# Kernel optimization log

Hardware: AMD Instinct MI355X
Metric: run time of the kernel (lower is better)

The kernel has to match this reference:

```python
import jax, jax.numpy as jnp
import numpy as np

HID = 32
NUM_GRAPHS = 256
N_NODES = 100000


def graph_conv(x, src, dst, ew, rel_w, rel_b, root_w):
    # PyG GraphConv: out = lin_rel(sum_{j in N(i)} e_ji * x_j) + lin_root(x_i)
    msg = x[src] * ew[:, None]                                  # [E, F] gather
    agg = jax.ops.segment_sum(msg, dst, num_segments=N_NODES)    # [N, F] scatter-add
    return agg @ rel_w + rel_b + x @ root_w


def setup_inputs() -> dict:
    key = jax.random.key(0)
    ks = jax.random.split(key, 16)
    N, E, F = N_NODES, 1600000, 64
    x = jax.random.normal(ks[0], (N, F), dtype=jnp.float32)
    edge_index = jax.random.randint(ks[1], (2, E), 0, N, dtype=jnp.int64)
    edge_attr = jax.random.uniform(ks[2], (E,), dtype=jnp.float32)
    batch = jnp.sort(jax.random.randint(ks[3], (N,), 0, NUM_GRAPHS, dtype=jnp.int64))
    s = lambda k, shp: jax.random.normal(k, shp, dtype=jnp.float32) * 0.1
    return {
        "x": x, "edge_index": edge_index, "edge_attr": edge_attr, "batch": batch,
        "conv1_rel_w": s(ks[4], (F, HID)), "conv1_rel_b": jnp.zeros((HID,), jnp.float32),
        "conv1_root_w": s(ks[5], (F, HID)),
        "conv2_rel_w": s(ks[6], (HID, HID)), "conv2_rel_b": jnp.zeros((HID,), jnp.float32),
        "conv2_root_w": s(ks[7], (HID, HID)),
        "lin1_w": s(ks[8], (HID, 32)), "lin1_b": jnp.zeros((32,), jnp.float32),
        "lin2_w": s(ks[9], (32, 16)), "lin2_b": jnp.zeros((16,), jnp.float32),
        "lin_w": s(ks[10], (16, 1)), "lin_b": jnp.zeros((1,), jnp.float32),
    }


def reference(x, edge_index, edge_attr, batch,
              conv1_rel_w, conv1_rel_b, conv1_root_w,
              conv2_rel_w, conv2_rel_b, conv2_root_w,
              lin1_w, lin1_b, lin2_w, lin2_b, lin_w, lin_b):
    src, dst = edge_index[0], edge_index[1]
    h = jax.nn.relu(graph_conv(x, src, dst, edge_attr, conv1_rel_w, conv1_rel_b, conv1_root_w))
    h = jax.nn.relu(graph_conv(h, src, dst, edge_attr, conv2_rel_w, conv2_rel_b, conv2_root_w))
    # global mean pool over graphs
    sums = jax.ops.segment_sum(h, batch, num_segments=NUM_GRAPHS)          # [G, 32]
    cnts = jax.ops.segment_sum(jnp.ones((h.shape[0],), h.dtype), batch, num_segments=NUM_GRAPHS)
    g = sums / jnp.maximum(cnts, 1.0)[:, None]
    # dropout is identity in eval mode
    g = jax.nn.relu(g @ lin1_w + lin1_b)
    g = g @ lin2_w + lin2_b
    g = jax.nn.relu(g)
    return g @ lin_w + lin_b  # [G, 1]
```

## Files before the change

kernel.cpp:

```cpp
#include <hip/hip_runtime.h>

#define NGRAPH 256
#define FIN 64
#define HID 32
#define NB_SHIFT 8
#define NB_NODES 256
#define KMAX2 512
#define EPB 2048
#define EPT 8
#define NT 64
#define XPAD 65
#define HPAD 33

__global__ __launch_bounds__(256, 4) void node_lin64(
    const float* __restrict__ x, const float* __restrict__ Wrel,
    const float* __restrict__ Wroot, const float* __restrict__ bias,
    float* __restrict__ A, float* __restrict__ B, int N)
{
    __shared__ float sWr[FIN * HID];
    __shared__ float sWo[FIN * HID];
    __shared__ float sb[HID];
    __shared__ float sx[NT * XPAD];
    int tid = threadIdx.x;
    {
        const float4* Wr4 = (const float4*)Wrel;
        const float4* Wo4 = (const float4*)Wroot;
        for (int i = tid; i < FIN * HID / 4; i += 256) {
            ((float4*)sWr)[i] = Wr4[i];
            ((float4*)sWo)[i] = Wo4[i];
        }
        if (tid < HID) sb[tid] = bias[tid];
    }
    int base = blockIdx.x * NT;
    {
        const float4* x4 = (const float4*)x;
        for (int i = tid; i < NT * 16; i += 256) {
            int row = i >> 4, c4 = i & 15;
            int n = base + row;
            float4 v = (n < N) ? x4[(size_t)n * 16 + c4]
                               : make_float4(0.f, 0.f, 0.f, 0.f);
            *(float4*)&sx[row * XPAD + c4 * 4] = v;
        }
    }
    __syncthreads();

    int nl = tid >> 3;
    int fq = (tid & 7) * 4;
    const float* xa = &sx[nl * XPAD];
    const float* xb = &sx[(nl + 32) * XPAD];
    float4 ar0 = make_float4(0.f,0.f,0.f,0.f), ao0 = ar0;
    float4 ar1 = ar0, ao1 = ar0;
    #pragma unroll 4
    for (int k = 0; k < FIN; ++k) {
        float4 w4 = *(const float4*)&sWr[k * HID + fq];
        float4 o4 = *(const float4*)&sWo[k * HID + fq];
        float va = xa[k], vb = xb[k];
        ar0.x = fmaf(va, w4.x, ar0.x); ar0.y = fmaf(va, w4.y, ar0.y);
        ar0.z = fmaf(va, w4.z, ar0.z); ar0.w = fmaf(va, w4.w, ar0.w);
        ao0.x = fmaf(va, o4.x, ao0.x); ao0.y = fmaf(va, o4.y, ao0.y);
        ao0.z = fmaf(va, o4.z, ao0.z); ao0.w = fmaf(va, o4.w, ao0.w);
        ar1.x = fmaf(vb, w4.x, ar1.x); ar1.y = fmaf(vb, w4.y, ar1.y);
        ar1.z = fmaf(vb, w4.z, ar1.z); ar1.w = fmaf(vb, w4.w, ar1.w);
        ao1.x = fmaf(vb, o4.x, ao1.x); ao1.y = fmaf(vb, o4.y, ao1.y);
        ao1.z = fmaf(vb, o4.z, ao1.z); ao1.w = fmaf(vb, o4.w, ao1.w);
    }
    float4 bb = *(const float4*)&sb[fq];
    int n0 = base + nl, n1 = base + nl + 32;
    if (n0 < N) {
        *(float4*)&A[(size_t)n0 * HID + fq] = ar0;
        ao0.x += bb.x; ao0.y += bb.y; ao0.z += bb.z; ao0.w += bb.w;
        *(float4*)&B[(size_t)n0 * HID + fq] = ao0;
    }
    if (n1 < N) {
        *(float4*)&A[(size_t)n1 * HID + fq] = ar1;
        ao1.x += bb.x; ao1.y += bb.y; ao1.z += bb.z; ao1.w += bb.w;
        *(float4*)&B[(size_t)n1 * HID + fq] = ao1;
    }
}

__global__ __launch_bounds__(256, 4) void node_lin32(
    const float* __restrict__ Hpre, const float* __restrict__ Wrel,
    const float* __restrict__ Wroot, const float* __restrict__ bias,
    float* __restrict__ A, float* __restrict__ C, int N)
{
    __shared__ float sWr[HID * HID];
    __shared__ float sWo[HID * HID];
    __shared__ float sb[HID];
    __shared__ float sh[NT * HPAD];
    int tid = threadIdx.x;
    {
        const float4* Wr4 = (const float4*)Wrel;
        const float4* Wo4 = (const float4*)Wroot;
        for (int i = tid; i < HID * HID / 4; i += 256) {
            ((float4*)sWr)[i] = Wr4[i];
            ((float4*)sWo)[i] = Wo4[i];
        }
        if (tid < HID) sb[tid] = bias[tid];
    }
    int base = blockIdx.x * NT;
    {
        const float4* H4 = (const float4*)Hpre;
        for (int i = tid; i < NT * 8; i += 256) {
            int row = i >> 3, c4 = i & 7;
            int n = base + row;
            float4 v = make_float4(0.f, 0.f, 0.f, 0.f);
            if (n < N) {
                v = H4[(size_t)n * 8 + c4];
                v.x = v.x > 0.f ? v.x : 0.f; v.y = v.y > 0.f ? v.y : 0.f;
                v.z = v.z > 0.f ? v.z : 0.f; v.w = v.w > 0.f ? v.w : 0.f;
            }
            *(float4*)&sh[row * HPAD + c4 * 4] = v;
        }
    }
    __syncthreads();

    int nl = tid >> 3;
    int fq = (tid & 7) * 4;
    const float* xa = &sh[nl * HPAD];
    const float* xb = &sh[(nl + 32) * HPAD];
    float4 ar0 = make_float4(0.f,0.f,0.f,0.f), ao0 = ar0;
    float4 ar1 = ar0, ao1 = ar0;
    #pragma unroll 4
    for (int k = 0; k < HID; ++k) {
        float4 w4 = *(const float4*)&sWr[k * HID + fq];
        float4 o4 = *(const float4*)&sWo[k * HID + fq];
        float va = xa[k], vb = xb[k];
        ar0.x = fmaf(va, w4.x, ar0.x); ar0.y = fmaf(va, w4.y, ar0.y);
        ar0.z = fmaf(va, w4.z, ar0.z); ar0.w = fmaf(va, w4.w, ar0.w);
        ao0.x = fmaf(va, o4.x, ao0.x); ao0.y = fmaf(va, o4.y, ao0.y);
        ao0.z = fmaf(va, o4.z, ao0.z); ao0.w = fmaf(va, o4.w, ao0.w);
        ar1.x = fmaf(vb, w4.x, ar1.x); ar1.y = fmaf(vb, w4.y, ar1.y);
        ar1.z = fmaf(vb, w4.z, ar1.z); ar1.w = fmaf(vb, w4.w, ar1.w);
        ao1.x = fmaf(vb, o4.x, ao1.x); ao1.y = fmaf(vb, o4.y, ao1.y);
        ao1.z = fmaf(vb, o4.z, ao1.z); ao1.w = fmaf(vb, o4.w, ao1.w);
    }
    float4 bb = *(const float4*)&sb[fq];
    int n0 = base + nl, n1 = base + nl + 32;
    if (n0 < N) {
        *(float4*)&A[(size_t)n0 * HID + fq] = ar0;
        ao0.x += bb.x; ao0.y += bb.y; ao0.z += bb.z; ao0.w += bb.w;
        *(float4*)&C[(size_t)n0 * HID + fq] = ao0;
    }
    if (n1 < N) {
        *(float4*)&A[(size_t)n1 * HID + fq] = ar1;
        ao1.x += bb.x; ao1.y += bb.y; ao1.z += bb.z; ao1.w += bb.w;
        *(float4*)&C[(size_t)n1 * HID + fq] = ao1;
    }
}


__global__ __launch_bounds__(256) void bucket_hist(
    const int* __restrict__ dst, int* __restrict__ cbb, int E, int K, int NBLK)
{
    __shared__ int h[KMAX2];
    int tid = threadIdx.x;
    for (int i = tid; i < K; i += 256) h[i] = 0;
    __syncthreads();
    int e0 = blockIdx.x * EPB + tid * 8;
    if (e0 + 7 < E) {
        int4 d0 = *reinterpret_cast<const int4*>(dst + e0);
        int4 d1 = *reinterpret_cast<const int4*>(dst + e0 + 4);
        atomicAdd(&h[d0.x >> NB_SHIFT], 1); atomicAdd(&h[d0.y >> NB_SHIFT], 1);
        atomicAdd(&h[d0.z >> NB_SHIFT], 1); atomicAdd(&h[d0.w >> NB_SHIFT], 1);
        atomicAdd(&h[d1.x >> NB_SHIFT], 1); atomicAdd(&h[d1.y >> NB_SHIFT], 1);
        atomicAdd(&h[d1.z >> NB_SHIFT], 1); atomicAdd(&h[d1.w >> NB_SHIFT], 1);
    } else {
        for (int e = e0; e < E && e < e0 + 8; ++e)
            atomicAdd(&h[dst[e] >> NB_SHIFT], 1);
    }
    __syncthreads();
    for (int i = tid; i < K; i += 256)
        cbb[(size_t)i * NBLK + blockIdx.x] = h[i];
}

__global__ __launch_bounds__(256) void bucket_scan(
    int* __restrict__ cbb, int* __restrict__ btot, int NBLK)
{
    __shared__ int sc[256];
    size_t row = (size_t)blockIdx.x * NBLK;
    int t = threadIdx.x;
    int base = t * 4;
    int v[4]; int s = 0;
    #pragma unroll
    for (int j = 0; j < 4; ++j) { v[j] = (base + j < NBLK) ? cbb[row + base + j] : 0; s += v[j]; }
    sc[t] = s;
    __syncthreads();
    int acc = s;
    for (int off = 1; off < 256; off <<= 1) {
        int add = (t >= off) ? sc[t - off] : 0;
        __syncthreads();
        acc += add;
        sc[t] = acc;
        __syncthreads();
    }
    int run = acc - s;
    #pragma unroll
    for (int j = 0; j < 4; ++j) {
        if (base + j < NBLK) cbb[row + base + j] = run;
        run += v[j];
    }
    if (t == 255) btot[blockIdx.x] = acc;
}

__global__ __launch_bounds__(256) void btot_scan(
    const int* __restrict__ btot, int* __restrict__ bbase, int K)
{
    __shared__ int sc[256];
    int t = threadIdx.x;
    int base = t * 4;
    int v[4]; int s = 0;
    #pragma unroll
    for (int j = 0; j < 4; ++j) { v[j] = (base + j < K) ? btot[base + j] : 0; s += v[j]; }
    sc[t] = s;
    __syncthreads();
    int acc = s;
    for (int off = 1; off < 256; off <<= 1) {
        int add = (t >= off) ? sc[t - off] : 0;
        __syncthreads();
        acc += add;
        sc[t] = acc;
        __syncthreads();
    }
    int run = acc - s;
    #pragma unroll
    for (int j = 0; j < 4; ++j) {
        if (base + j < K) bbase[base + j] = run;
        run += v[j];
    }
    if (t == 255) bbase[K] = acc;
}

__global__ __launch_bounds__(256) void partB(
    const int* __restrict__ src, const int* __restrict__ dst,
    const float* __restrict__ ew, const int* __restrict__ cbb,
    const int* __restrict__ bbase, int2* __restrict__ stg8,
    int E, int K, int NBLK)
{
    __shared__ int4 pay[EPB];
    __shared__ int h[KMAX2];
    __shared__ int lofs[KMAX2];
    __shared__ int gb[KMAX2];
    __shared__ int sc[256];
    int tid = threadIdx.x;
    for (int i = tid; i < K; i += 256) h[i] = 0;
    __syncthreads();

    int base = blockIdx.x * EPB;
    int es[EPT], ds[EPT]; float wsr[EPT];
    #pragma unroll
    for (int k = 0; k < EPT; ++k) {
        int e = base + k * 256 + tid;
        if (e < E) {
            es[k] = src[e]; ds[k] = dst[e]; wsr[k] = ew[e];
            atomicAdd(&h[ds[k] >> NB_SHIFT], 1);
        } else ds[k] = -1;
    }
    __syncthreads();

    int b0 = tid * 2;
    int v0 = (b0 < K) ? h[b0] : 0;
    int v1 = (b0 + 1 < K) ? h[b0 + 1] : 0;
    int s = v0 + v1;
    sc[tid] = s;
    __syncthreads();
    int acc = s;
    for (int off = 1; off < 256; off <<= 1) {
        int add = (tid >= off) ? sc[tid - off] : 0;
        __syncthreads();
        acc += add;
        sc[tid] = acc;
        __syncthreads();
    }
    int run = acc - s;
    if (b0 < K) lofs[b0] = run;
    if (b0 + 1 < K) lofs[b0 + 1] = run + v0;
    __syncthreads();

    for (int b = tid; b < K; b += 256) {
        gb[b] = bbase[b] + cbb[(size_t)b * NBLK + blockIdx.x];
        h[b] = lofs[b];
    }
    __syncthreads();

    #pragma unroll
    for (int k = 0; k < EPT; ++k) {
        if (ds[k] >= 0) {
            int b = ds[k] >> NB_SHIFT;
            int dloc = ds[k] & (NB_NODES - 1);
            int slot = atomicAdd(&h[b], 1);
            pay[slot] = make_int4(es[k] | (dloc << 17), __float_as_int(wsr[k]),
                                  gb[b] + slot - lofs[b], 0);
        }
    }
    __syncthreads();

    int tot = E - base; if (tot > EPB) tot = EPB;
    for (int i = tid; i < tot; i += 256) {
        int4 p = pay[i];
        stg8[p.z] = make_int2(p.x, p.y);
    }
}

__global__ __launch_bounds__(512) void partC2(
    const int2* __restrict__ stg8, const int* __restrict__ bbase,
    int* __restrict__ rowptr, int2* __restrict__ perm, int N, int K)
{
    __shared__ int hcnt[NB_NODES];
    __shared__ int hinc[NB_NODES];
    int b = blockIdx.x;
    int n0 = b << NB_SHIFT;
    int nTop = n0 + NB_NODES; if (nTop > N) nTop = N;
    int nloc = nTop - n0;
    int tid = threadIdx.x;
    if (tid < NB_NODES) hcnt[tid] = 0;
    __syncthreads();
    int lo = bbase[b], hi = bbase[b + 1];
    for (int e = lo + tid; e < hi; e += 512)
        atomicAdd(&hcnt[stg8[e].x >> 17], 1);
    __syncthreads();
    if (tid < NB_NODES) hinc[tid] = hcnt[tid];
    __syncthreads();
    for (int off = 1; off < NB_NODES; off <<= 1) {
        int v = (tid < NB_NODES && tid >= off) ? hinc[tid - off] : 0;
        __syncthreads();
        if (tid < NB_NODES) hinc[tid] += v;
        __syncthreads();
    }
    if (tid < nloc) {
        int excl = hinc[tid] - hcnt[tid];
        rowptr[n0 + tid] = lo + excl;
        hcnt[tid] = excl;
    }
    if (b == K - 1 && tid == 0) rowptr[N] = hi;
    __syncthreads();
    for (int e = lo + tid; e < hi; e += 512) {
        int2 p = stg8[e];
        int pos = lo + atomicAdd(&hcnt[p.x >> 17], 1);
        perm[pos] = make_int2(p.x & 0x1FFFF, p.y);
    }
}

__global__ __launch_bounds__(256) void csr_agg(
    const int* __restrict__ rowptr, const int2* __restrict__ perm,
    const float* __restrict__ A, float* __restrict__ out, int N)
{
    int gid = blockIdx.x * 256 + threadIdx.x;
    int n = gid >> 6;
    if (n >= N) return;
    int lane = threadIdx.x & 63;
    int slot = lane >> 3;
    int q = lane & 7;
    int e0 = rowptr[n], e1 = rowptr[n + 1];
    const float4* A4 = (const float4*)A;
    float4 a0 = make_float4(0.f, 0.f, 0.f, 0.f);
    float4 a1 = make_float4(0.f, 0.f, 0.f, 0.f);
    int e = e0 + slot;
    for (; e + 8 < e1; e += 16) {
        int2 p0 = perm[e];
        int2 p1 = perm[e + 8];
        float4 v0 = A4[(size_t)p0.x * 8 + q];
        float4 v1 = A4[(size_t)p1.x * 8 + q];
        float w0 = __int_as_float(p0.y), w1 = __int_as_float(p1.y);
        a0.x = fmaf(v0.x, w0, a0.x); a0.y = fmaf(v0.y, w0, a0.y);
        a0.z = fmaf(v0.z, w0, a0.z); a0.w = fmaf(v0.w, w0, a0.w);
        a1.x = fmaf(v1.x, w1, a1.x); a1.y = fmaf(v1.y, w1, a1.y);
        a1.z = fmaf(v1.z, w1, a1.z); a1.w = fmaf(v1.w, w1, a1.w);
    }
    for (; e < e1; e += 8) {
        int2 p = perm[e];
        float4 v = A4[(size_t)p.x * 8 + q];
        float w = __int_as_float(p.y);
        a0.x = fmaf(v.x, w, a0.x); a0.y = fmaf(v.y, w, a0.y);
        a0.z = fmaf(v.z, w, a0.z); a0.w = fmaf(v.w, w, a0.w);
    }
    a0.x += a1.x; a0.y += a1.y; a0.z += a1.z; a0.w += a1.w;
    #pragma unroll
    for (int off = 8; off < 64; off <<= 1) {
        a0.x += __shfl_xor(a0.x, off, 64);
        a0.y += __shfl_xor(a0.y, off, 64);
        a0.z += __shfl_xor(a0.z, off, 64);
        a0.w += __shfl_xor(a0.w, off, 64);
    }
    if (lane < 8) {
        float4* O4 = (float4*)out;
        size_t oi = (size_t)n * 8 + q;
        float4 o = O4[oi];
        o.x += a0.x; o.y += a0.y; o.z += a0.z; o.w += a0.w;
        O4[oi] = o;
    }
}

__global__ __launch_bounds__(256) void pool_kernel(
    const float* __restrict__ C, const int* __restrict__ batch,
    float* __restrict__ sums, float* __restrict__ cnts, int N)
{
    int f = threadIdx.x & 31, g = threadIdx.x >> 5;
    int n0 = blockIdx.x * 256 + g * 32;
    if (n0 >= N) return;
    int n1 = n0 + 32; if (n1 > N) n1 = N;
    int cur = batch[n0];
    float acc = 0.f, cnt = 0.f;
    for (int n = n0; n < n1; ++n) {
        int b = batch[n];
        if (b != cur) {
            atomicAdd(&sums[cur * HID + f], acc);
            if (f == 0) atomicAdd(&cnts[cur], cnt);
            acc = 0.f; cnt = 0.f; cur = b;
        }
        float v = C[(size_t)n * HID + f];
        acc += v > 0.f ? v : 0.f;
        cnt += 1.f;
    }
    atomicAdd(&sums[cur * HID + f], acc);
    if (f == 0) atomicAdd(&cnts[cur], cnt);
}

__global__ __launch_bounds__(256) void mlp_kernel(
    const float* __restrict__ sums, const float* __restrict__ cnts,
    const float* __restrict__ W1, const float* __restrict__ b1,
    const float* __restrict__ W2, const float* __restrict__ b2,
    const float* __restrict__ W3, const float* __restrict__ b3,
    float* __restrict__ out)
{
    __shared__ float sW1[32 * 32], sb1[32], sW2[32 * 16], sb2[16], sW3[16], sb3;
    int tid = threadIdx.x;
    for (int i = tid; i < 32 * 32; i += 256) sW1[i] = W1[i];
    for (int i = tid; i < 32 * 16; i += 256) sW2[i] = W2[i];
    if (tid < 32) sb1[tid] = b1[tid];
    if (tid < 16) { sb2[tid] = b2[tid]; sW3[tid] = W3[tid]; }
    if (tid == 0) sb3 = b3[0];
    __syncthreads();
    int gi = tid;
    float c = cnts[gi]; c = c > 1.f ? c : 1.f;
    float inv = 1.f / c;
    float gvec[32];
    #pragma unroll
    for (int i = 0; i < 32; ++i) gvec[i] = sums[gi * 32 + i] * inv;
    float h1[32];
    #pragma unroll
    for (int j = 0; j < 32; ++j) {
        float a = sb1[j];
        #pragma unroll
        for (int k = 0; k < 32; ++k) a = fmaf(gvec[k], sW1[k * 32 + j], a);
        h1[j] = a > 0.f ? a : 0.f;
    }
    float o = sb3;
    #pragma unroll
    for (int j = 0; j < 16; ++j) {
        float a = sb2[j];
        #pragma unroll
        for (int k = 0; k < 32; ++k) a = fmaf(h1[k], sW2[k * 16 + j], a);
        a = a > 0.f ? a : 0.f;
        o = fmaf(a, sW3[j], o);
    }
    out[gi] = o;
}

extern "C" void kernel_launch(void* const* d_in, const int* in_sizes, int n_in,
                              void* d_out, int out_size, void* d_ws, size_t ws_size,
                              hipStream_t stream) {
    const float* x     = (const float*)d_in[0];
    const int*   ei    = (const int*)d_in[1];
    const float* ew    = (const float*)d_in[2];
    const int*   batch = (const int*)d_in[3];
    const float* c1rw  = (const float*)d_in[4];
    const float* c1rb  = (const float*)d_in[5];
    const float* c1ow  = (const float*)d_in[6];
    const float* c2rw  = (const float*)d_in[7];
    const float* c2rb  = (const float*)d_in[8];
    const float* c2ow  = (const float*)d_in[9];
    const float* l1w   = (const float*)d_in[10];
    const float* l1b   = (const float*)d_in[11];
    const float* l2w   = (const float*)d_in[12];
    const float* l2b   = (const float*)d_in[13];
    const float* lw    = (const float*)d_in[14];
    const float* lb    = (const float*)d_in[15];

    int N = in_sizes[0] / FIN;
    int E = in_sizes[2];
    const int* src = ei;
    const int* dst = ei + E;
    int K    = (N + NB_NODES - 1) >> NB_SHIFT;
    int NBLK = (E + EPB - 1) / EPB;

    char* ws = (char*)d_ws;
    size_t off = 0;
    auto alloc = [&](size_t nbytes) { void* p = ws + off; off += (nbytes + 255) & ~size_t(255); return p; };
    float* A      = (float*)alloc((size_t)N * HID * 4);
    float* BC     = (float*)alloc((size_t)N * HID * 4);
    int2*  perm   = (int2*) alloc((size_t)E * 8);
    int*   rowptr = (int*)  alloc((size_t)(N + 1) * 4);
    int*   btot   = (int*)  alloc((size_t)KMAX2 * 4);
    int*   bbase  = (int*)  alloc((size_t)(KMAX2 + 1) * 4);
    float* sums   = (float*)alloc(NGRAPH * HID * 4);
    float* cnts   = (float*)alloc(NGRAPH * 4);
    int*   cbb    = (int*)A;
    int2*  stg8   = (int2*)BC;

    hipMemsetAsync(sums, 0, (NGRAPH * HID + NGRAPH) * 4, stream);

    int nb_node = (N + NT - 1) / NT;
    int nb_agg  = (int)(((long long)N * 64 + 255) / 256);

    bucket_hist<<<NBLK, 256, 0, stream>>>(dst, cbb, E, K, NBLK);
    bucket_scan<<<K, 256, 0, stream>>>(cbb, btot, NBLK);
    btot_scan<<<1, 256, 0, stream>>>(btot, bbase, K);
    partB<<<NBLK, 256, 0, stream>>>(src, dst, ew, cbb, bbase, stg8, E, K, NBLK);
    partC2<<<K, 512, 0, stream>>>(stg8, bbase, rowptr, perm, N, K);

    node_lin64<<<nb_node, 256, 0, stream>>>(x, c1rw, c1ow, c1rb, A, BC, N);
    csr_agg<<<nb_agg, 256, 0, stream>>>(rowptr, perm, A, BC, N);
    node_lin32<<<nb_node, 256, 0, stream>>>(BC, c2rw, c2ow, c2rb, A, BC, N);
    csr_agg<<<nb_agg, 256, 0, stream>>>(rowptr, perm, A, BC, N);
    pool_kernel<<<(N + 255) / 256, 256, 0, stream>>>(BC, batch, sums, cnts, N);
    mlp_kernel<<<1, 256, 0, stream>>>(sums, cnts, l1w, l1b, l2w, l2b, lw, lb,
                                      (float*)d_out);
}
```

Measured before the change: 187.1 us.

## Fuse mean pooling and MLP into one per-graph kernel using binary search on sorted batch

Replaces the atomic-based pool kernel, the memset, and the single-block MLP kernel with one kernel that runs one block per graph. Each block binary-searches the sorted batch array to find its node range, reduces the relu'd features in shared memory, then evaluates the small MLP. This removes a memset, a launch and all global atomics, but relies on batch being sorted and gives the pooling only 256 blocks of parallelism.

```diff
diff --git a/kernel.cpp b/kernel.cpp
--- a/kernel.cpp
+++ b/kernel.cpp
@@ -390,70 +390,64 @@
     }
 }
 
-__global__ __launch_bounds__(256) void pool_kernel(
-    const float* __restrict__ C, const int* __restrict__ batch,
-    float* __restrict__ sums, float* __restrict__ cnts, int N)
-{
-    int f = threadIdx.x & 31, g = threadIdx.x >> 5;
-    int n0 = blockIdx.x * 256 + g * 32;
-    if (n0 >= N) return;
-    int n1 = n0 + 32; if (n1 > N) n1 = N;
-    int cur = batch[n0];
-    float acc = 0.f, cnt = 0.f;
-    for (int n = n0; n < n1; ++n) {
-        int b = batch[n];
-        if (b != cur) {
-            atomicAdd(&sums[cur * HID + f], acc);
-            if (f == 0) atomicAdd(&cnts[cur], cnt);
-            acc = 0.f; cnt = 0.f; cur = b;
-        }
-        float v = C[(size_t)n * HID + f];
-        acc += v > 0.f ? v : 0.f;
-        cnt += 1.f;
-    }
-    atomicAdd(&sums[cur * HID + f], acc);
-    if (f == 0) atomicAdd(&cnts[cur], cnt);
-}
-
-__global__ __launch_bounds__(256) void mlp_kernel(
-    const float* __restrict__ sums, const float* __restrict__ cnts,
+__global__ __launch_bounds__(256) void pool_mlp(
+    const float* __restrict__ C, const int* __restrict__ batch, int N,
     const float* __restrict__ W1, const float* __restrict__ b1,
     const float* __restrict__ W2, const float* __restrict__ b2,
     const float* __restrict__ W3, const float* __restrict__ b3,
     float* __restrict__ out)
 {
-    __shared__ float sW1[32 * 32], sb1[32], sW2[32 * 16], sb2[16], sW3[16], sb3;
+    int g = blockIdx.x;
     int tid = threadIdx.x;
-    for (int i = tid; i < 32 * 32; i += 256) sW1[i] = W1[i];
-    for (int i = tid; i < 32 * 16; i += 256) sW2[i] = W2[i];
-    if (tid < 32) sb1[tid] = b1[tid];
-    if (tid < 16) { sb2[tid] = b2[tid]; sW3[tid] = W3[tid]; }
-    if (tid == 0) sb3 = b3[0];
-    __syncthreads();
-    int gi = tid;
-    float c = cnts[gi]; c = c > 1.f ? c : 1.f;
-    float inv = 1.f / c;
-    float gvec[32];
-    #pragma unroll
-    for (int i = 0; i < 32; ++i) gvec[i] = sums[gi * 32 + i] * inv;
-    float h1[32];
-    #pragma unroll
-    for (int j = 0; j < 32; ++j) {
-        float a = sb1[j];
+    int lo, hi;
+    {
+        int l = 0, r = N;
+        while (l < r) { int m = (l + r) >> 1; if (batch[m] < g) l = m + 1; else r = m; }
+        lo = l;
+        r = N;
+        while (l < r) { int m = (l + r) >> 1; if (batch[m] < g + 1) l = m + 1; else r = m; }
+        hi = l;
+    }
+    __shared__ float ssum[8][32];
+    __shared__ float gvec[32];
+    __shared__ float h1v[32];
+    __shared__ float h2v[16];
+    int f = tid & 31, seg = tid >> 5;
+    float acc = 0.f;
+    for (int n = lo + seg; n < hi; n += 8) {
+        float v = C[(size_t)n * HID + f];
+        acc += v > 0.f ? v : 0.f;
+    }
+    ssum[seg][f] = acc;
+    __syncthreads();
+    if (tid < 32) {
+        float s = 0.f;
         #pragma unroll
-        for (int k = 0; k < 32; ++k) a = fmaf(gvec[k], sW1[k * 32 + j], a);
-        h1[j] = a > 0.f ? a : 0.f;
-    }
-    float o = sb3;
-    #pragma unroll
-    for (int j = 0; j < 16; ++j) {
-        float a = sb2[j];
+        for (int k = 0; k < 8; ++k) s += ssum[k][tid];
+        float c = (float)(hi - lo); c = c > 1.f ? c : 1.f;
+        gvec[tid] = s / c;
+    }
+    __syncthreads();
+    if (tid < 32) {
+        float a = b1[tid];
         #pragma unroll
-        for (int k = 0; k < 32; ++k) a = fmaf(h1[k], sW2[k * 16 + j], a);
-        a = a > 0.f ? a : 0.f;
-        o = fmaf(a, sW3[j], o);
-    }
-    out[gi] = o;
+        for (int k = 0; k < 32; ++k) a = fmaf(gvec[k], W1[k * 32 + tid], a);
+        h1v[tid] = a > 0.f ? a : 0.f;
+    }
+    __syncthreads();
+    if (tid < 16) {
+        float a = b2[tid];
+        #pragma unroll
+        for (int k = 0; k < 32; ++k) a = fmaf(h1v[k], W2[k * 16 + tid], a);
+        h2v[tid] = a > 0.f ? a : 0.f;
+    }
+    __syncthreads();
+    if (tid == 0) {
+        float o = b3[0];
+        #pragma unroll
+        for (int k = 0; k < 16; ++k) o = fmaf(h2v[k], W3[k], o);
+        out[g] = o;
+    }
 }
 
 extern "C" void kernel_launch(void* const* d_in, const int* in_sizes, int n_in,
@@ -492,12 +486,8 @@
     int*   rowptr = (int*)  alloc((size_t)(N + 1) * 4);
     int*   btot   = (int*)  alloc((size_t)KMAX2 * 4);
     int*   bbase  = (int*)  alloc((size_t)(KMAX2 + 1) * 4);
-    float* sums   = (float*)alloc(NGRAPH * HID * 4);
-    float* cnts   = (float*)alloc(NGRAPH * 4);
     int*   cbb    = (int*)A;
     int2*  stg8   = (int2*)BC;
-
-    hipMemsetAsync(sums, 0, (NGRAPH * HID + NGRAPH) * 4, stream);
 
     int nb_node = (N + NT - 1) / NT;
     int nb_agg  = (int)(((long long)N * 64 + 255) / 256);
@@ -512,7 +502,6 @@
     csr_agg<<<nb_agg, 256, 0, stream>>>(rowptr, perm, A, BC, N);
     node_lin32<<<nb_node, 256, 0, stream>>>(BC, c2rw, c2ow, c2rb, A, BC, N);
     csr_agg<<<nb_agg, 256, 0, stream>>>(rowptr, perm, A, BC, N);
-    pool_kernel<<<(N + 255) / 256, 256, 0, stream>>>(BC, batch, sums, cnts, N);
-    mlp_kernel<<<1, 256, 0, stream>>>(sums, cnts, l1w, l1b, l2w, l2b, lw, lb,
-                                      (float*)d_out);
-}
+    pool_mlp<<<NGRAPH, 256, 0, stream>>>(BC, batch, N, l1w, l1b, l2w, l2b, lw, lb,
+                                         (float*)d_out);
+}
```

After: 176.8 us. 5.5% less time.
